# Optimization experiments

Measured on AMD Instinct MI355X. Metric: run time of the kernel, lower is better.

## Reference

```python
import jax, jax.numpy as jnp
import numpy as np

B, L, S, LA, NA, E, D, H, NHID = 16, 256, 100, 48, 32, 64, 768, 12, 1024
W_IDX = S + 2
EPS = 1e-12


def setup_inputs() -> dict:
    rng = np.random.default_rng(0)
    key = jax.random.key(0)
    ks = jax.random.split(key, 8)
    idxs = np.zeros((B, W_IDX), dtype=np.int64)
    bert_lens = np.zeros((B,), dtype=np.int64)
    is_trig = np.zeros((B, S), dtype=np.float32)
    ent_map = np.zeros((B, S, E), dtype=np.float32)
    argw_mask = np.zeros((B, LA, 1), dtype=np.float32)
    for b in range(B):
        sb = int(rng.integers(60, S + 1))          # n first-subword tokens
        ab = int(rng.integers(8, LA + 1))          # n arg-role subwords
        sent_idx = np.sort(rng.choice(np.arange(1, 2 * sb + 1), size=sb, replace=False))
        sls = 2 * sb + 1                           # second-to-last [SEP] position
        last = sls + ab + 1                        # last [SEP] position
        idxs[b, :sb] = sent_idx
        idxs[b, sb] = sls
        idxs[b, sb + 1] = last
        bert_lens[b] = last + 1
        t0 = int(rng.integers(0, sb - 1))
        is_trig[b, t0:t0 + 2] = 1.0
        eb = int(rng.integers(16, E + 1))
        for e in range(eb):
            ent_map[b, int(rng.integers(0, sb)), e] = 1.0
        argw_mask[b, :ab, 0] = 1.0
    arg_w = np.asarray(jax.random.uniform(ks[0], (B, LA, NA), dtype=jnp.float32)) * argw_mask
    return {
        'all_embeddings': jax.random.normal(ks[1], (B, L, D), dtype=jnp.float32),
        'is_triggers': jnp.asarray(is_trig),
        'arg_weight_matrices': jnp.asarray(arg_w, dtype=jnp.float32),
        'entity_mapping': jnp.asarray(ent_map),
        'att0': jax.random.uniform(ks[2], (B, H, L, L), dtype=jnp.float32),
        'att1': jax.random.uniform(ks[3], (B, H, L, L), dtype=jnp.float32),
        'att2': jax.random.uniform(ks[4], (B, H, L, L), dtype=jnp.float32),
        'W_ta': jax.random.normal(ks[5], (3 * D, D), dtype=jnp.float32) * 0.02,
        'b_ta': jnp.zeros((D,), dtype=jnp.float32),
        'W1': jax.random.normal(ks[6], (6 * D, NHID), dtype=jnp.float32) * 0.02,
        'b1': jnp.zeros((NHID,), dtype=jnp.float32),
        'W2': jax.random.normal(ks[7], (NHID, 1), dtype=jnp.float32) * 0.02,
        'b2': jnp.zeros((1,), dtype=jnp.float32),
        'idxs_to_collect': jnp.asarray(idxs),
        'bert_sentence_lengths': jnp.asarray(bert_lens),
    }


def _l1_normalize(x, axis):
    # F.normalize(x, p=1, dim=axis)
    return x / jnp.clip(jnp.sum(jnp.abs(x), axis=axis, keepdims=True), EPS)


def reference(all_embeddings, is_triggers, arg_weight_matrices, entity_mapping,
              att0, att1, att2, W_ta, b_ta, W1, b1, W2, b2,
              idxs_to_collect, bert_sentence_lengths):
    idxs = idxs_to_collect
    valid = idxs > 0                                   # [B,W]
    n_valid = jnp.sum(valid, axis=1)                   # [B]
    j = jnp.arange(S)
    sent_valid = (j[None, :] < (n_valid - 2)[:, None]).astype(all_embeddings.dtype)  # [B,S]
    sent_idx = idxs[:, :S]
    # first-subword gather, zero-padded (get_fist_subword_embeddings)
    sent_emb = jnp.take_along_axis(all_embeddings, sent_idx[:, :, None], axis=1) * sent_valid[:, :, None]
    # arg-role segment: (second_last_sep+1) .. (bert_len-2), zero-padded to LA
    sls = jnp.take_along_axis(idxs, (n_valid - 2)[:, None], axis=1)[:, 0]   # [B]
    arg_pos = sls[:, None] + 1 + jnp.arange(LA)[None, :]                    # [B,LA]
    arg_valid = (arg_pos < (bert_sentence_lengths - 1)[:, None]).astype(all_embeddings.dtype)
    arg_emb0 = jnp.take_along_axis(all_embeddings, jnp.clip(arg_pos, 0, L - 1)[:, :, None], axis=1) * arg_valid[:, :, None]
    # entity aggregation + trigger mean pooling
    entity = jnp.einsum('bsd,bse->bed', sent_emb, entity_mapping)           # [B,E,D]
    trig = jnp.sum(sent_emb * is_triggers[:, :, None], axis=1) / jnp.sum(is_triggers, axis=1)[:, None]
    arg = jnp.einsum('bld,bla->bad', arg_emb0, arg_weight_matrices)         # [B,NA,D]
    # trigger-aware entity fusion
    trig_e = jnp.broadcast_to(trig[:, None, :], entity.shape)
    nonempty = (jnp.sum(jnp.abs(entity), axis=-1) > 0).astype(entity.dtype)
    ent_cat = jnp.concatenate([entity, trig_e, entity * trig_e], axis=-1)   # [B,E,3D]
    entity = (ent_cat @ W_ta + b_ta) * nonempty[:, :, None]
    # bidirectional token<->arg attention (L1-normalized)
    score = jnp.einsum('bed,bad->bea', entity, arg) / np.sqrt(D)            # [B,E,NA]
    t2a = _l1_normalize(score, 2)[..., None]
    a2t = _l1_normalize(score, 1)[..., None]
    token_argAwared = jnp.sum(arg[:, None] * t2a, axis=2)                   # [B,E,D]
    arg_tokenAwared = jnp.sum(entity[:, :, None] * a2t, axis=1)             # [B,NA,D]
    # select_hidden_att: head-mean, gather collected rows/cols, row-renormalize
    def sel_att(att):
        m = jnp.mean(att, axis=1)                                           # [B,L,L]
        r = jnp.take_along_axis(m, sent_idx[:, :, None], axis=1)            # [B,S,L]
        c = jnp.take_along_axis(r, sent_idx[:, None, :], axis=2)            # [B,S,S]
        c = c * sent_valid[:, :, None] * sent_valid[:, None, :]
        return c / jnp.clip(jnp.sum(c, axis=-1, keepdims=True), EPS)
    t2t = (sel_att(att0) + sel_att(att1) + sel_att(att2)) / 3.0             # [B,S,S]
    a_h2h_tok = t2t @ sent_emb                                              # [B,S,D]
    A_h2h = jnp.einsum('bse,bsd->bed', entity_mapping, a_h2h_tok)           # [B,E,D]
    H_ = jnp.einsum('bse,bsd->bed', entity_mapping, sent_emb)               # [B,E,D]
    a2a = jax.nn.softmax(arg @ jnp.swapaxes(arg, -1, -2), axis=-1)
    A_u2u = a2a @ arg                                                       # [B,NA,D]
    shp = (B, E, NA, D)
    latent = jnp.concatenate([
        jnp.broadcast_to(H_[:, :, None], shp),
        jnp.broadcast_to(arg[:, None], shp),
        jnp.broadcast_to(token_argAwared[:, :, None], shp),
        jnp.broadcast_to(A_h2h[:, :, None], shp),
        jnp.broadcast_to(arg_tokenAwared[:, None], shp),
        jnp.broadcast_to(A_u2u[:, None], shp),
    ], axis=-1)                                                             # [B,E,NA,6D]
    h = jax.nn.gelu(latent @ W1 + b1, approximate=False)
    out = (h @ W2 + b2)[..., 0]                                             # [B,E,NA]
    return out
```

## Files before the change

kernel.cpp:

```cpp
#include <hip/hip_runtime.h>
#include <math.h>

#define B_ 16
#define L_ 256
#define S_ 100
#define LA_ 48
#define NA_ 32
#define E_ 64
#define D_ 768
#define H_ 12
#define NHID_ 1024
#define WIDX_ 102
#define EPSF 1e-12f

typedef __attribute__((ext_vector_type(8))) short s16x8;
typedef __attribute__((ext_vector_type(4))) float f32x4;

__device__ __forceinline__ void split_bf16(float x, unsigned short& h, unsigned short& l) {
  unsigned u = __float_as_uint(x);
  unsigned hr = u + 0x7FFFu + ((u >> 16) & 1u);
  h = (unsigned short)(hr >> 16);
  float r = x - __uint_as_float(hr & 0xFFFF0000u);
  unsigned u2 = __float_as_uint(r);
  unsigned lr = u2 + 0x7FFFu + ((u2 >> 16) & 1u);
  l = (unsigned short)(lr >> 16);
}

__global__ void k_meta(const int* __restrict__ idxs, const int* __restrict__ blen,
                       int* __restrict__ meta) {
  int b = blockIdx.x, t = threadIdx.x;
  __shared__ int cnt;
  if (t == 0) cnt = 0;
  __syncthreads();
  if (t < WIDX_ && idxs[b * WIDX_ + t] > 0) atomicAdd(&cnt, 1);
  __syncthreads();
  if (t == 0) {
    int sb = cnt - 2;
    meta[b * 4 + 0] = sb;
    meta[b * 4 + 1] = idxs[b * WIDX_ + sb];
    meta[b * 4 + 2] = blen[b] - 1;
  }
}

__global__ void k_gather(const float* __restrict__ emb, const int* __restrict__ idxs,
                         const int* __restrict__ meta, float* __restrict__ sent_emb,
                         float* __restrict__ arg_emb) {
  int b = blockIdx.y, y = blockIdx.x, t = threadIdx.x;
  int sb = meta[b * 4 + 0], sls = meta[b * 4 + 1], last = meta[b * 4 + 2];
  if (y < S_) {
    int s = y;
    float* dst = sent_emb + ((size_t)b * S_ + s) * D_;
    if (s < sb) {
      const float* src = emb + ((size_t)b * L_ + idxs[b * WIDX_ + s]) * D_;
      for (int d = t; d < D_; d += 256) dst[d] = src[d];
    } else {
      for (int d = t; d < D_; d += 256) dst[d] = 0.f;
    }
  } else {
    int l = y - S_;
    int pos = sls + 1 + l;
    float* dst = arg_emb + ((size_t)b * LA_ + l) * D_;
    if (pos < last) {
      int p = pos > (L_ - 1) ? (L_ - 1) : pos;
      const float* src = emb + ((size_t)b * L_ + p) * D_;
      for (int d = t; d < D_; d += 256) dst[d] = src[d];
    } else {
      for (int d = t; d < D_; d += 256) dst[d] = 0.f;
    }
  }
}

__global__ void k_trig(const float* __restrict__ sent_emb, const float* __restrict__ is_trig,
                       float* __restrict__ trig) {
  int b = blockIdx.y;
  int d = blockIdx.x * 256 + threadIdx.x;
  float acc = 0.f, den = 0.f;
  for (int s = 0; s < S_; s++) {
    float w = is_trig[b * S_ + s];
    den += w;
    if (w != 0.f) acc += w * sent_emb[((size_t)b * S_ + s) * D_ + d];
  }
  trig[b * D_ + d] = acc / den;
}

__global__ __launch_bounds__(256) void k_entity0(const float* __restrict__ sent_emb,
                                                 const float* __restrict__ ent_map,
                                                 const float* __restrict__ trig,
                                                 unsigned short* __restrict__ e0h,
                                                 unsigned short* __restrict__ e0l,
                                                 unsigned short* __restrict__ e0th,
                                                 unsigned short* __restrict__ e0tl,
                                                 float* __restrict__ ne) {
  int b = blockIdx.y, e = blockIdx.x, t = threadIdx.x;
  float a0 = 0.f, a1 = 0.f, a2 = 0.f;
  for (int s = 0; s < S_; s++) {
    float w = ent_map[((size_t)b * S_ + s) * E_ + e];
    if (w != 0.f) {
      const float* r = sent_emb + ((size_t)b * S_ + s) * D_;
      a0 += w * r[t]; a1 += w * r[t + 256]; a2 += w * r[t + 512];
    }
  }
  size_t o = ((size_t)b * E_ + e) * D_;
  const float* tr = trig + b * D_;
  unsigned short h, lo;
  split_bf16(a0, h, lo); e0h[o + t] = h; e0l[o + t] = lo;
  split_bf16(a1, h, lo); e0h[o + t + 256] = h; e0l[o + t + 256] = lo;
  split_bf16(a2, h, lo); e0h[o + t + 512] = h; e0l[o + t + 512] = lo;
  split_bf16(a0 * tr[t], h, lo); e0th[o + t] = h; e0tl[o + t] = lo;
  split_bf16(a1 * tr[t + 256], h, lo); e0th[o + t + 256] = h; e0tl[o + t + 256] = lo;
  split_bf16(a2 * tr[t + 512], h, lo); e0th[o + t + 512] = h; e0tl[o + t + 512] = lo;
  __shared__ float red[256];
  red[t] = fabsf(a0) + fabsf(a1) + fabsf(a2);
  __syncthreads();
  for (int s2 = 128; s2 > 0; s2 >>= 1) {
    if (t < s2) red[t] += red[t + s2];
    __syncthreads();
  }
  if (t == 0) ne[b * E_ + e] = (red[0] > 0.f) ? 1.f : 0.f;
}

__global__ __launch_bounds__(256) void k_wsum(const float* __restrict__ Wm, int wstride, int sy,
                                              int sx, const float* __restrict__ Vm,
                                              float* __restrict__ Om,
                                              unsigned short* __restrict__ oh,
                                              unsigned short* __restrict__ ol, int Y) {
  int b = blockIdx.y, x = blockIdx.x, t = threadIdx.x;
  float a0 = 0.f, a1 = 0.f, a2 = 0.f;
  const float* wb = Wm + (size_t)b * wstride + (size_t)x * sx;
  const float* vb = Vm + (size_t)b * Y * D_;
  for (int y = 0; y < Y; y++) {
    float w = wb[(size_t)y * sy];
    if (w != 0.f) {
      const float* r = vb + (size_t)y * D_;
      a0 += w * r[t]; a1 += w * r[t + 256]; a2 += w * r[t + 512];
    }
  }
  size_t oidx = ((size_t)b * gridDim.x + x) * D_;
  if (Om) {
    Om[oidx + t] = a0; Om[oidx + t + 256] = a1; Om[oidx + t + 512] = a2;
  }
  if (oh) {
    unsigned short h, lo;
    split_bf16(a0, h, lo); oh[oidx + t] = h; ol[oidx + t] = lo;
    split_bf16(a1, h, lo); oh[oidx + t + 256] = h; ol[oidx + t + 256] = lo;
    split_bf16(a2, h, lo); oh[oidx + t + 512] = h; ol[oidx + t + 512] = lo;
  }
}

__global__ void k_tb(const float* __restrict__ trig, const float* __restrict__ W_ta,
                     const float* __restrict__ b_ta, float* __restrict__ tb) {
  int b = blockIdx.y;
  int d = blockIdx.x * 256 + threadIdx.x;
  float acc0 = b_ta[d], acc1 = 0.f, acc2 = 0.f, acc3 = 0.f;
  float acc4 = 0.f, acc5 = 0.f, acc6 = 0.f, acc7 = 0.f;
  const float* tr = trig + b * D_;
  const float* w = W_ta + (size_t)D_ * D_ + d;
  for (int k = 0; k < D_; k += 8) {
    acc0 += tr[k + 0] * w[(size_t)(k + 0) * D_];
    acc1 += tr[k + 1] * w[(size_t)(k + 1) * D_];
    acc2 += tr[k + 2] * w[(size_t)(k + 2) * D_];
    acc3 += tr[k + 3] * w[(size_t)(k + 3) * D_];
    acc4 += tr[k + 4] * w[(size_t)(k + 4) * D_];
    acc5 += tr[k + 5] * w[(size_t)(k + 5) * D_];
    acc6 += tr[k + 6] * w[(size_t)(k + 6) * D_];
    acc7 += tr[k + 7] * w[(size_t)(k + 7) * D_];
  }
  tb[b * D_ + d] = ((acc0 + acc1) + (acc2 + acc3)) + ((acc4 + acc5) + (acc6 + acc7));
}

__global__ __launch_bounds__(256) void k_cvtT(const float* __restrict__ src, int K, int N,
                                              unsigned short* __restrict__ th,
                                              unsigned short* __restrict__ tl) {
  __shared__ float tile[32][33];
  int k0 = blockIdx.x * 32, n0 = blockIdx.y * 32;
  int tr = threadIdx.x >> 3, c4 = (threadIdx.x & 7) * 4;
  float4 v = *(const float4*)(src + (size_t)(k0 + tr) * N + n0 + c4);
  tile[tr][c4] = v.x; tile[tr][c4 + 1] = v.y; tile[tr][c4 + 2] = v.z; tile[tr][c4 + 3] = v.w;
  __syncthreads();
  unsigned short h[4], l[4];
#pragma unroll
  for (int i = 0; i < 4; ++i) split_bf16(tile[c4 + i][tr], h[i], l[i]);
  size_t oo = (size_t)(n0 + tr) * K + k0 + c4;
  th[oo + 0] = h[0]; th[oo + 1] = h[1]; th[oo + 2] = h[2]; th[oo + 3] = h[3];
  tl[oo + 0] = l[0]; tl[oo + 1] = l[1]; tl[oo + 2] = l[2]; tl[oo + 3] = l[3];
}

__global__ __launch_bounds__(256) void k_mgemm(
    int phase,
    const unsigned short* __restrict__ e0h, const unsigned short* __restrict__ e0l,
    const unsigned short* __restrict__ e0th, const unsigned short* __restrict__ e0tl,
    const unsigned short* __restrict__ Ah2hh, const unsigned short* __restrict__ Ah2hl,
    const unsigned short* __restrict__ argmh, const unsigned short* __restrict__ argml,
    const unsigned short* __restrict__ Au2uh, const unsigned short* __restrict__ Au2ul,
    const unsigned short* __restrict__ entnh, const unsigned short* __restrict__ entnl,
    const unsigned short* __restrict__ WtaTh, const unsigned short* __restrict__ WtaTl,
    const unsigned short* __restrict__ W1Th, const unsigned short* __restrict__ W1Tl,
    float* __restrict__ Cpe, float* __restrict__ PeAp, float* __restrict__ PaAp,
    float* __restrict__ P2, float* __restrict__ Q2) {
  const size_t HPE = (size_t)B_ * E_ * NHID_;
  const size_t HPA = (size_t)B_ * NA_ * NHID_;
  const size_t HH = (size_t)1024 * 768;
  int flat = blockIdx.x;
  int xcd = flat & 7;
  int i = flat >> 3;
  int by8 = i & 7;
  int colIdx = i >> 3;
  int job, bx, byTop = 0;
  if (phase == 0) {
    int gc = xcd * 20 + colIdx;
    if (gc < 24)       { job = 0; int r = gc;       bx = r >> 1; byTop = (r & 1) << 3; }
    else if (gc < 48)  { job = 1; int r = gc - 24;  bx = r >> 1; byTop = (r & 1) << 3; }
    else if (gc < 80)  { job = 2; int r = gc - 48;  bx = r >> 1; byTop = (r & 1) << 3; }
    else if (gc < 112) { job = 3; int r = gc - 80;  bx = r >> 1; byTop = (r & 1) << 3; }
    else if (gc < 128) { job = 4; bx = gc - 112; }
    else if (gc < 144) { job = 5; bx = gc - 128; }
    else               { job = 6; bx = gc - 144; }
  } else {
    int gc = xcd * 4 + colIdx;
    job = 7; bx = gc >> 1; byTop = (gc & 1) << 3;
  }
  int by = byTop + by8;

  const unsigned short *Ah_, *Al_, *Bh_, *Bl_;
  float* C;
  int bstride, N, bkoff;
  switch (job) {
    case 0: Ah_ = e0h;   Al_ = e0l;   Bh_ = WtaTh; Bl_ = WtaTl; bstride = 2304;
            bkoff = 0;        C = Cpe;        N = 768;  break;
    case 1: Ah_ = e0th;  Al_ = e0tl;  Bh_ = WtaTh; Bl_ = WtaTl; bstride = 2304;
            bkoff = 1536;     C = Cpe + HH;   N = 768;  break;
    case 2: Ah_ = e0h;   Al_ = e0l;   Bh_ = W1Th;  Bl_ = W1Tl;  bstride = 4608;
            bkoff = 0;        C = PeAp;       N = 1024; break;
    case 3: Ah_ = Ah2hh; Al_ = Ah2hl; Bh_ = W1Th;  Bl_ = W1Tl;  bstride = 4608;
            bkoff = 3 * 768;  C = PeAp + HPE; N = 1024; break;
    case 4: Ah_ = argmh; Al_ = argml; Bh_ = W1Th;  Bl_ = W1Tl;  bstride = 4608;
            bkoff = 768;      C = PaAp;       N = 1024; break;
    case 5: Ah_ = Au2uh; Al_ = Au2ul; Bh_ = W1Th;  Bl_ = W1Tl;  bstride = 4608;
            bkoff = 5 * 768;  C = PaAp + HPA; N = 1024; break;
    case 6: Ah_ = argmh; Al_ = argml; Bh_ = W1Th;  Bl_ = W1Tl;  bstride = 4608;
            bkoff = 2 * 768;  C = P2;         N = 1024; break;
    default: Ah_ = entnh; Al_ = entnl; Bh_ = W1Th; Bl_ = W1Tl;  bstride = 4608;
            bkoff = 4 * 768;  C = Q2;         N = 1024; break;
  }

  __shared__ unsigned short As[2][2][64][4][8];
  __shared__ unsigned short Bs[2][2][64][4][8];

  int tid = threadIdx.x;
  int srow = tid >> 2, sg = tid & 3;
  int wc = sg ^ ((srow >> 1) & 3);
  const unsigned short* aPh = Ah_ + (size_t)(by * 64 + srow) * 768 + sg * 8;
  const unsigned short* aPl = Al_ + (size_t)(by * 64 + srow) * 768 + sg * 8;
  const unsigned short* bPh = Bh_ + (size_t)(bx * 64 + srow) * bstride + bkoff + sg * 8;
  const unsigned short* bPl = Bl_ + (size_t)(bx * 64 + srow) * bstride + bkoff + sg * 8;

  int lane = tid & 63, wave = tid >> 6;
  int wm = wave >> 1, wn = wave & 1;
  int fg = lane >> 4, fr = lane & 15;
  int ar0 = wm * 32 + fr;
  int bc0 = wn * 32 + fr;
  int ca = fg ^ ((ar0 >> 1) & 3);
  int cb = fg ^ ((bc0 >> 1) & 3);

  f32x4 acc00 = {0.f, 0.f, 0.f, 0.f}, acc01 = {0.f, 0.f, 0.f, 0.f};
  f32x4 acc10 = {0.f, 0.f, 0.f, 0.f}, acc11 = {0.f, 0.f, 0.f, 0.f};

  const int niter = 24;
  s16x8 a0h = *(const s16x8*)(aPh + 0), a0l = *(const s16x8*)(aPl + 0);
  s16x8 b0h = *(const s16x8*)(bPh + 0), b0l = *(const s16x8*)(bPl + 0);
  s16x8 a1h = *(const s16x8*)(aPh + 32), a1l = *(const s16x8*)(aPl + 32);
  s16x8 b1h = *(const s16x8*)(bPh + 32), b1l = *(const s16x8*)(bPl + 32);

#define WRITE_LDS(buf, ah, al, bh, bl)              \
  {                                                 \
    *(s16x8*)&As[buf][0][srow][wc][0] = ah;         \
    *(s16x8*)&As[buf][1][srow][wc][0] = al;         \
    *(s16x8*)&Bs[buf][0][srow][wc][0] = bh;         \
    *(s16x8*)&Bs[buf][1][srow][wc][0] = bl;         \
  }
#define LOAD_SET(ah, al, bh, bl, t_)                \
  {                                                 \
    ah = *(const s16x8*)(aPh + (t_) * 32);          \
    al = *(const s16x8*)(aPl + (t_) * 32);          \
    bh = *(const s16x8*)(bPh + (t_) * 32);          \
    bl = *(const s16x8*)(bPl + (t_) * 32);          \
  }
#define READ_MFMA(buf)                                                          \
  {                                                                             \
    s16x8 xah0 = *(const s16x8*)&As[buf][0][ar0][ca][0];                        \
    s16x8 xah1 = *(const s16x8*)&As[buf][0][ar0 + 16][ca][0];                   \
    s16x8 xal0 = *(const s16x8*)&As[buf][1][ar0][ca][0];                        \
    s16x8 xal1 = *(const s16x8*)&As[buf][1][ar0 + 16][ca][0];                   \
    s16x8 xbh0 = *(const s16x8*)&Bs[buf][0][bc0][cb][0];                        \
    s16x8 xbh1 = *(const s16x8*)&Bs[buf][0][bc0 + 16][cb][0];                   \
    s16x8 xbl0 = *(const s16x8*)&Bs[buf][1][bc0][cb][0];                        \
    s16x8 xbl1 = *(const s16x8*)&Bs[buf][1][bc0 + 16][cb][0];                   \
    acc00 = __builtin_amdgcn_mfma_f32_16x16x32_bf16(xah0, xbh0, acc00, 0, 0, 0); \
    acc00 = __builtin_amdgcn_mfma_f32_16x16x32_bf16(xah0, xbl0, acc00, 0, 0, 0); \
    acc00 = __builtin_amdgcn_mfma_f32_16x16x32_bf16(xal0, xbh0, acc00, 0, 0, 0); \
    acc01 = __builtin_amdgcn_mfma_f32_16x16x32_bf16(xah0, xbh1, acc01, 0, 0, 0); \
    acc01 = __builtin_amdgcn_mfma_f32_16x16x32_bf16(xah0, xbl1, acc01, 0, 0, 0); \
    acc01 = __builtin_amdgcn_mfma_f32_16x16x32_bf16(xal0, xbh1, acc01, 0, 0, 0); \
    acc10 = __builtin_amdgcn_mfma_f32_16x16x32_bf16(xah1, xbh0, acc10, 0, 0, 0); \
    acc10 = __builtin_amdgcn_mfma_f32_16x16x32_bf16(xah1, xbl0, acc10, 0, 0, 0); \
    acc10 = __builtin_amdgcn_mfma_f32_16x16x32_bf16(xal1, xbh0, acc10, 0, 0, 0); \
    acc11 = __builtin_amdgcn_mfma_f32_16x16x32_bf16(xah1, xbh1, acc11, 0, 0, 0); \
    acc11 = __builtin_amdgcn_mfma_f32_16x16x32_bf16(xah1, xbl1, acc11, 0, 0, 0); \
    acc11 = __builtin_amdgcn_mfma_f32_16x16x32_bf16(xal1, xbh1, acc11, 0, 0, 0); \
  }

  WRITE_LDS(0, a0h, a0l, b0h, b0l);
  LOAD_SET(a0h, a0l, b0h, b0l, 2);
  __syncthreads();

  for (int it = 0; it < niter; it += 2) {
    if (it + 1 < niter) {
      WRITE_LDS(1, a1h, a1l, b1h, b1l);
      if (it + 3 < niter) LOAD_SET(a1h, a1l, b1h, b1l, it + 3);
    }
    READ_MFMA(0);
    __syncthreads();
    if (it + 2 < niter) {
      WRITE_LDS(0, a0h, a0l, b0h, b0l);
      if (it + 4 < niter) LOAD_SET(a0h, a0l, b0h, b0l, it + 4);
    }
    READ_MFMA(1);
    __syncthreads();
  }
#undef WRITE_LDS
#undef LOAD_SET
#undef READ_MFMA

  f32x4 accs[2][2] = {{acc00, acc01}, {acc10, acc11}};
  int colb = bx * 64 + wn * 32 + fr;
  int rowb = by * 64 + wm * 32 + fg * 4;
#pragma unroll
  for (int i2 = 0; i2 < 2; ++i2) {
#pragma unroll
    for (int j = 0; j < 2; ++j) {
      int col = colb + j * 16;
#pragma unroll
      for (int r = 0; r < 4; ++r) {
        int row = rowb + i2 * 16 + r;
        C[(size_t)row * N + col] = accs[i2][j][r];
      }
    }
  }
}

__global__ __launch_bounds__(256) void k_combE(const float* __restrict__ Cpe,
                                               const float* __restrict__ tb,
                                               const float* __restrict__ ne,
                                               float* __restrict__ entn,
                                               unsigned short* __restrict__ entnh,
                                               unsigned short* __restrict__ entnl) {
  int t = threadIdx.x;
  int r0 = blockIdx.x * 4;
  const size_t HH = (size_t)1024 * 768;
#pragma unroll
  for (int i = 0; i < 4; ++i) {
    int row = r0 + i;
    int b = row >> 6;
    float nev = ne[row];
#pragma unroll
    for (int j = 0; j < 3; ++j) {
      int col = t + j * 256;
      size_t o = (size_t)row * D_ + col;
      float v = (Cpe[o] + Cpe[HH + o] + tb[(size_t)b * D_ + col]) * nev;
      entn[o] = v;
      unsigned short hh, ll;
      split_bf16(v, hh, ll);
      entnh[o] = hh; entnl[o] = ll;
    }
  }
}

__global__ __launch_bounds__(256) void k_score(const float* __restrict__ entn,
                                               const float* __restrict__ argm,
                                               float* __restrict__ score) {
  int b = blockIdx.y, e = blockIdx.x, t = threadIdx.x;
  __shared__ float ent[D_];
  const float* er = entn + ((size_t)b * E_ + e) * D_;
  for (int d = t; d < D_; d += 256) ent[d] = er[d];
  __syncthreads();
  int wave = t >> 6, lane = t & 63;
  const float scale = 0.03608439182435161f;
  for (int a = wave; a < NA_; a += 4) {
    const float* ar = argm + ((size_t)b * NA_ + a) * D_;
    float p = 0.f;
#pragma unroll
    for (int i = 0; i < 12; i++) {
      int d = lane + 64 * i;
      p += ent[d] * ar[d];
    }
    for (int off = 32; off > 0; off >>= 1) p += __shfl_down(p, off);
    if (lane == 0) score[((size_t)b * E_ + e) * NA_ + a] = p * scale;
  }
}

__global__ __launch_bounds__(256) void k_a2a(const float* __restrict__ argm,
                                             float* __restrict__ a2a) {
  int b = blockIdx.y, a = blockIdx.x, t = threadIdx.x;
  __shared__ float sA[D_];
  __shared__ float lg[NA_];
  const float* ar = argm + ((size_t)b * NA_ + a) * D_;
  for (int d = t; d < D_; d += 256) sA[d] = ar[d];
  __syncthreads();
  int wave = t >> 6, lane = t & 63;
  for (int a2 = wave; a2 < NA_; a2 += 4) {
    const float* br = argm + ((size_t)b * NA_ + a2) * D_;
    float p = 0.f;
#pragma unroll
    for (int i = 0; i < 12; i++) {
      int d = lane + 64 * i;
      p += sA[d] * br[d];
    }
    for (int off = 32; off > 0; off >>= 1) p += __shfl_down(p, off);
    if (lane == 0) lg[a2] = p;
  }
  __syncthreads();
  if (t < 64) {
    float v = (t < NA_) ? lg[t] : -INFINITY;
    float m = v;
    for (int mask = 16; mask > 0; mask >>= 1) m = fmaxf(m, __shfl_xor(m, mask));
    float ex = (t < NA_) ? expf(v - m) : 0.f;
    float sm = ex;
    for (int mask = 16; mask > 0; mask >>= 1) sm += __shfl_xor(sm, mask);
    if (t < NA_) a2a[((size_t)b * NA_ + a) * NA_ + t] = ex / sm;
  }
}

__global__ __launch_bounds__(128) void k_t2t(const float* __restrict__ att0,
                                             const float* __restrict__ att1,
                                             const float* __restrict__ att2,
                                             const int* __restrict__ idxs,
                                             const int* __restrict__ meta,
                                             float* __restrict__ t2t) {
  int b = blockIdx.y, s = blockIdx.x, t = threadIdx.x;
  int sb = meta[b * 4 + 0];
  float* out = t2t + ((size_t)b * S_ + s) * S_;
  if (s >= sb) {
    for (int j = t; j < S_; j += 128) out[j] = 0.f;
    return;
  }
  int Is = idxs[b * WIDX_ + s];
  int It = (t < S_) ? idxs[b * WIDX_ + t] : 0;
  __shared__ float row[256];
  __shared__ float red[128];
  const float* atts[3] = {att0, att1, att2};
  float accout = 0.f;
  for (int q = 0; q < 3; q++) {
    float r0 = 0.f, r1 = 0.f;
    const float* base = atts[q] + (((size_t)b * H_) * L_ + Is) * L_;
    for (int h = 0; h < H_; h++) {
      const float* rp = base + (size_t)h * L_ * L_;
      r0 += rp[t];
      r1 += rp[t + 128];
    }
    row[t] = r0;
    row[t + 128] = r1;
    __syncthreads();
    float v = (t < sb) ? row[It] * (1.f / 12.f) : 0.f;
    red[t] = v;
    __syncthreads();
    for (int s2 = 64; s2 > 0; s2 >>= 1) {
      if (t < s2) red[t] += red[t + s2];
      __syncthreads();
    }
    float rsum = red[0];
    __syncthreads();
    accout += v / fmaxf(rsum, EPSF) * (1.f / 3.f);
  }
  if (t < S_) out[t] = accout;
}

__global__ __launch_bounds__(256) void k_mix(const float* __restrict__ PeAp,
                                             const float* __restrict__ PaAp,
                                             const float* __restrict__ P2,
                                             const float* __restrict__ Q2,
                                             const float* __restrict__ score,
                                             const float* __restrict__ b1,
                                             float* __restrict__ ps, float* __restrict__ qs) {
  int b = blockIdx.y, x = blockIdx.x, t = threadIdx.x;
  int n0 = t * 4;
  const size_t HPE = (size_t)B_ * E_ * NHID_;
  const size_t HPA = (size_t)B_ * NA_ * NHID_;
  __shared__ float sc[E_];
  if (x < E_) {
    int e = x;
    size_t ro = ((size_t)b * E_ + e) * NHID_ + n0;
    float4 acc = *(const float4*)(PeAp + ro);
    float4 u1 = *(const float4*)(PeAp + HPE + ro);
    float4 bb = *(const float4*)(b1 + n0);
    acc.x += u1.x + bb.x; acc.y += u1.y + bb.y;
    acc.z += u1.z + bb.z; acc.w += u1.w + bb.w;
    if (t < NA_) sc[t] = score[((size_t)b * E_ + e) * NA_ + t];
    __syncthreads();
    float rs = 0.f;
    for (int a = 0; a < NA_; a++) rs += fabsf(sc[a]);
    rs = fmaxf(rs, EPSF);
    const float* pb = P2 + (size_t)b * NA_ * NHID_ + n0;
#pragma unroll 2
    for (int a = 0; a < NA_; a++) {
      float ww = sc[a] / rs;
      float4 p = *(const float4*)(pb + (size_t)a * NHID_);
      acc.x += ww * p.x; acc.y += ww * p.y; acc.z += ww * p.z; acc.w += ww * p.w;
    }
    *(float4*)(ps + ro) = acc;
  } else {
    int a = x - E_;
    size_t ro = ((size_t)b * NA_ + a) * NHID_ + n0;
    float4 acc = *(const float4*)(PaAp + ro);
    float4 u1 = *(const float4*)(PaAp + HPA + ro);
    acc.x += u1.x; acc.y += u1.y; acc.z += u1.z; acc.w += u1.w;
    if (t < E_) sc[t] = score[((size_t)b * E_ + t) * NA_ + a];
    __syncthreads();
    float cs = 0.f;
    for (int e = 0; e < E_; e++) cs += fabsf(sc[e]);
    cs = fmaxf(cs, EPSF);
    const float* qb = Q2 + (size_t)b * E_ * NHID_ + n0;
#pragma unroll 2
    for (int e = 0; e < E_; e++) {
      float ww = sc[e] / cs;
      float4 q = *(const float4*)(qb + (size_t)e * NHID_);
      acc.x += ww * q.x; acc.y += ww * q.y; acc.z += ww * q.z; acc.w += ww * q.w;
    }
    *(float4*)(qs + ro) = acc;
  }
}

__global__ __launch_bounds__(256) void k_final(const float* __restrict__ ps,
                                               const float* __restrict__ qs,
                                               const float* __restrict__ W2,
                                               const float* __restrict__ b2,
                                               float* __restrict__ out) {
  int b = blockIdx.y, e = blockIdx.x, t = threadIdx.x;
  int wave = t >> 6, lane = t & 63;
  const float ks = 0.70710678118654752f;
  size_t po = ((size_t)b * E_ + e) * NHID_ + lane * 4;
  float4 p0 = *(const float4*)(ps + po);
  float4 p1 = *(const float4*)(ps + po + 256);
  float4 p2 = *(const float4*)(ps + po + 512);
  float4 p3 = *(const float4*)(ps + po + 768);
  const float* w2p = W2 + lane * 4;
  float4 w0 = *(const float4*)(w2p);
  float4 w1 = *(const float4*)(w2p + 256);
  float4 w2 = *(const float4*)(w2p + 512);
  float4 w3 = *(const float4*)(w2p + 768);
  __shared__ float outs[NA_];
#pragma unroll 2
  for (int a = wave; a < NA_; a += 4) {
    size_t qo = ((size_t)b * NA_ + a) * NHID_ + lane * 4;
    float4 q0 = *(const float4*)(qs + qo);
    float4 q1 = *(const float4*)(qs + qo + 256);
    float4 q2 = *(const float4*)(qs + qo + 512);
    float4 q3 = *(const float4*)(qs + qo + 768);
    float acc = 0.f;
#define GEL4(pp, qq, ww)                                          \
    {                                                             \
      float x0 = pp.x + qq.x, x1 = pp.y + qq.y;                   \
      float x2 = pp.z + qq.z, x3 = pp.w + qq.w;                   \
      float g0 = 0.5f * x0 * (1.f + erff(x0 * ks));               \
      float g1 = 0.5f * x1 * (1.f + erff(x1 * ks));               \
      float g2 = 0.5f * x2 * (1.f + erff(x2 * ks));               \
      float g3 = 0.5f * x3 * (1.f + erff(x3 * ks));               \
      acc += g0 * ww.x + g1 * ww.y + g2 * ww.z + g3 * ww.w;       \
    }
    GEL4(p0, q0, w0)
    GEL4(p1, q1, w1)
    GEL4(p2, q2, w2)
    GEL4(p3, q3, w3)
#undef GEL4
    acc += __shfl_xor(acc, 32);
    acc += __shfl_xor(acc, 16);
    acc += __shfl_xor(acc, 8);
    acc += __shfl_xor(acc, 4);
    acc += __shfl_xor(acc, 2);
    acc += __shfl_xor(acc, 1);
    if (lane == 0) outs[a] = acc;
  }
  __syncthreads();
  if (t < NA_) out[((size_t)b * E_ + e) * NA_ + t] = outs[t] + b2[0];
}

extern "C" void kernel_launch(void* const* d_in, const int* in_sizes, int n_in,
                              void* d_out, int out_size, void* d_ws, size_t ws_size,
                              hipStream_t stream) {
  const float* emb    = (const float*)d_in[0];
  const float* istrig = (const float*)d_in[1];
  const float* argw   = (const float*)d_in[2];
  const float* entmap = (const float*)d_in[3];
  const float* att0   = (const float*)d_in[4];
  const float* att1   = (const float*)d_in[5];
  const float* att2   = (const float*)d_in[6];
  const float* W_ta   = (const float*)d_in[7];
  const float* b_ta   = (const float*)d_in[8];
  const float* W1     = (const float*)d_in[9];
  const float* b1     = (const float*)d_in[10];
  const float* W2     = (const float*)d_in[11];
  const float* b2     = (const float*)d_in[12];
  const int*   idxs   = (const int*)d_in[13];
  const int*   blen   = (const int*)d_in[14];
  float* out = (float*)d_out;

  float* ws = (float*)d_ws;
  size_t o = 0;
  int* meta = (int*)ws; o += 256;
  float* sent_emb = ws + o; o += (size_t)B_ * S_ * D_;
  float* arg_emb  = ws + o; o += (size_t)B_ * LA_ * D_;
  float* trig     = ws + o; o += (size_t)B_ * D_;
  float* argm     = ws + o; o += (size_t)B_ * NA_ * D_;
  float* entn     = ws + o; o += (size_t)B_ * E_ * D_;
  float* tb       = ws + o; o += (size_t)B_ * D_;
  float* ne       = ws + o; o += (size_t)B_ * E_;
  float* score    = ws + o; o += (size_t)B_ * E_ * NA_;
  float* t2t      = ws + o; o += (size_t)B_ * S_ * S_;
  float* ah2h     = ws + o; o += (size_t)B_ * S_ * D_;
  float* a2a      = ws + o; o += (size_t)B_ * NA_ * NA_;
  float* Cpe      = ws + o; o += (size_t)2 * 1024 * 768;
  float* PeAp     = ws + o; o += (size_t)2 * B_ * E_ * NHID_;
  float* PaAp     = ws + o; o += (size_t)2 * B_ * NA_ * NHID_;
  float* P2       = ws + o; o += (size_t)B_ * NA_ * NHID_;
  float* Q2       = ws + o; o += (size_t)B_ * E_ * NHID_;
  float* ps = sent_emb;
  float* qs = arg_emb;

  o = (o + 3) & ~(size_t)3;
  unsigned short* us = (unsigned short*)(ws + o);
  size_t uo = 0;
  unsigned short* e0h   = us + uo; uo += (size_t)B_ * E_ * D_;
  unsigned short* e0l   = us + uo; uo += (size_t)B_ * E_ * D_;
  unsigned short* e0th  = us + uo; uo += (size_t)B_ * E_ * D_;
  unsigned short* e0tl  = us + uo; uo += (size_t)B_ * E_ * D_;
  unsigned short* Ah2hh = us + uo; uo += (size_t)B_ * E_ * D_;
  unsigned short* Ah2hl = us + uo; uo += (size_t)B_ * E_ * D_;
  unsigned short* argmh = us + uo; uo += (size_t)B_ * NA_ * D_;
  unsigned short* argml = us + uo; uo += (size_t)B_ * NA_ * D_;
  unsigned short* Au2uh = us + uo; uo += (size_t)B_ * NA_ * D_;
  unsigned short* Au2ul = us + uo; uo += (size_t)B_ * NA_ * D_;
  unsigned short* entnh = us + uo; uo += (size_t)B_ * E_ * D_;
  unsigned short* entnl = us + uo; uo += (size_t)B_ * E_ * D_;
  unsigned short* WtaTh = us + uo; uo += (size_t)2304 * 768;
  unsigned short* WtaTl = us + uo; uo += (size_t)2304 * 768;
  unsigned short* W1Th  = us + uo; uo += (size_t)4608 * 1024;
  unsigned short* W1Tl  = us + uo; uo += (size_t)4608 * 1024;

  k_meta<<<B_, 128, 0, stream>>>(idxs, blen, meta);
  k_cvtT<<<dim3(2304 / 32, 768 / 32), 256, 0, stream>>>(W_ta, 2304, 768, WtaTh, WtaTl);
  k_cvtT<<<dim3(4608 / 32, 1024 / 32), 256, 0, stream>>>(W1, 4608, 1024, W1Th, W1Tl);
  k_gather<<<dim3(S_ + LA_, B_), 256, 0, stream>>>(emb, idxs, meta, sent_emb, arg_emb);
  k_trig<<<dim3(3, B_), 256, 0, stream>>>(sent_emb, istrig, trig);
  k_entity0<<<dim3(E_, B_), 256, 0, stream>>>(sent_emb, entmap, trig, e0h, e0l, e0th, e0tl, ne);
  k_wsum<<<dim3(NA_, B_), 256, 0, stream>>>(argw, LA_ * NA_, NA_, 1, arg_emb, argm, argmh,
                                            argml, LA_);
  k_tb<<<dim3(3, B_), 256, 0, stream>>>(trig, W_ta, b_ta, tb);
  k_t2t<<<dim3(S_, B_), 128, 0, stream>>>(att0, att1, att2, idxs, meta, t2t);
  k_wsum<<<dim3(S_, B_), 256, 0, stream>>>(t2t, S_ * S_, 1, S_, sent_emb, ah2h, nullptr,
                                           nullptr, S_);
  k_wsum<<<dim3(E_, B_), 256, 0, stream>>>(entmap, S_ * E_, E_, 1, ah2h, nullptr, Ah2hh,
                                           Ah2hl, S_);
  k_a2a<<<dim3(NA_, B_), 256, 0, stream>>>(argm, a2a);
  k_wsum<<<dim3(NA_, B_), 256, 0, stream>>>(a2a, NA_ * NA_, 1, NA_, argm, nullptr, Au2uh,
                                            Au2ul, NA_);

  k_mgemm<<<dim3(1280), 256, 0, stream>>>(0, e0h, e0l, e0th, e0tl, Ah2hh, Ah2hl, argmh,
                                          argml, Au2uh, Au2ul, entnh, entnl, WtaTh, WtaTl,
                                          W1Th, W1Tl, Cpe, PeAp, PaAp, P2, Q2);

  k_combE<<<dim3(B_ * E_ / 4), 256, 0, stream>>>(Cpe, tb, ne, entn, entnh, entnl);

  k_mgemm<<<dim3(256), 256, 0, stream>>>(1, e0h, e0l, e0th, e0tl, Ah2hh, Ah2hl, argmh,
                                         argml, Au2uh, Au2ul, entnh, entnl, WtaTh, WtaTl,
                                         W1Th, W1Tl, Cpe, PeAp, PaAp, P2, Q2);

  k_score<<<dim3(E_, B_), 256, 0, stream>>>(entn, argm, score);
  k_mix<<<dim3(E_ + NA_, B_), 256, 0, stream>>>(PeAp, PaAp, P2, Q2, score, b1, ps, qs);

  k_final<<<dim3(E_, B_), 256, 0, stream>>>(ps, qs, W2, b2, out);
}
```

Before: 491.0 us.

## Enlarge mgemm tiles to 128x128 and split-K the phase-1 GEMM

The split-bf16 MFMA GEMM kernel moves from 64x64 tiles, with four 16x16 accumulators per wave, to 128x128 tiles with a 4x4 accumulator grid per wave. This raises data reuse per LDS load and cuts the phase-0 grid from 1280 blocks to 320. Phase 1 (entity GEMM) is split along K into two halves written to separate buffers, which k_mix now sums, so the small phase-1 grid still has 128 blocks. The costs are more registers and LDS per block (launch_bounds asks for 2 blocks/CU), fewer blocks to fill the GPU, and an extra Q2 buffer and read.

```diff
diff --git a/kernel.cpp b/kernel.cpp
--- a/kernel.cpp
+++ b/kernel.cpp
@@ -185,7 +185,7 @@
   tl[oo + 0] = l[0]; tl[oo + 1] = l[1]; tl[oo + 2] = l[2]; tl[oo + 3] = l[3];
 }
 
-__global__ __launch_bounds__(256) void k_mgemm(
+__global__ __launch_bounds__(256, 2) void k_mgemm(
     int phase,
     const unsigned short* __restrict__ e0h, const unsigned short* __restrict__ e0l,
     const unsigned short* __restrict__ e0th, const unsigned short* __restrict__ e0tl,
@@ -203,146 +203,152 @@
   int flat = blockIdx.x;
   int xcd = flat & 7;
   int i = flat >> 3;
-  int by8 = i & 7;
-  int colIdx = i >> 3;
-  int job, bx, byTop = 0;
-  if (phase == 0) {
-    int gc = xcd * 20 + colIdx;
-    if (gc < 24)       { job = 0; int r = gc;       bx = r >> 1; byTop = (r & 1) << 3; }
-    else if (gc < 48)  { job = 1; int r = gc - 24;  bx = r >> 1; byTop = (r & 1) << 3; }
-    else if (gc < 80)  { job = 2; int r = gc - 48;  bx = r >> 1; byTop = (r & 1) << 3; }
-    else if (gc < 112) { job = 3; int r = gc - 80;  bx = r >> 1; byTop = (r & 1) << 3; }
-    else if (gc < 128) { job = 4; bx = gc - 112; }
-    else if (gc < 144) { job = 5; bx = gc - 128; }
-    else               { job = 6; bx = gc - 144; }
-  } else {
-    int gc = xcd * 4 + colIdx;
-    job = 7; bx = gc >> 1; byTop = (gc & 1) << 3;
-  }
-  int by = byTop + by8;
-
+  int by4 = i & 3;
+  int seg = i >> 2;
+  int job, bx, byTop = 0, akoff = 0, niter, bkoff, bstride, N;
   const unsigned short *Ah_, *Al_, *Bh_, *Bl_;
   float* C;
-  int bstride, N, bkoff;
-  switch (job) {
-    case 0: Ah_ = e0h;   Al_ = e0l;   Bh_ = WtaTh; Bl_ = WtaTl; bstride = 2304;
-            bkoff = 0;        C = Cpe;        N = 768;  break;
-    case 1: Ah_ = e0th;  Al_ = e0tl;  Bh_ = WtaTh; Bl_ = WtaTl; bstride = 2304;
-            bkoff = 1536;     C = Cpe + HH;   N = 768;  break;
-    case 2: Ah_ = e0h;   Al_ = e0l;   Bh_ = W1Th;  Bl_ = W1Tl;  bstride = 4608;
-            bkoff = 0;        C = PeAp;       N = 1024; break;
-    case 3: Ah_ = Ah2hh; Al_ = Ah2hl; Bh_ = W1Th;  Bl_ = W1Tl;  bstride = 4608;
-            bkoff = 3 * 768;  C = PeAp + HPE; N = 1024; break;
-    case 4: Ah_ = argmh; Al_ = argml; Bh_ = W1Th;  Bl_ = W1Tl;  bstride = 4608;
-            bkoff = 768;      C = PaAp;       N = 1024; break;
-    case 5: Ah_ = Au2uh; Al_ = Au2ul; Bh_ = W1Th;  Bl_ = W1Tl;  bstride = 4608;
-            bkoff = 5 * 768;  C = PaAp + HPA; N = 1024; break;
-    case 6: Ah_ = argmh; Al_ = argml; Bh_ = W1Th;  Bl_ = W1Tl;  bstride = 4608;
-            bkoff = 2 * 768;  C = P2;         N = 1024; break;
-    default: Ah_ = entnh; Al_ = entnl; Bh_ = W1Th; Bl_ = W1Tl;  bstride = 4608;
-            bkoff = 4 * 768;  C = Q2;         N = 1024; break;
-  }
-
-  __shared__ unsigned short As[2][2][64][4][8];
-  __shared__ unsigned short Bs[2][2][64][4][8];
+  if (phase == 0) {
+    int gseg = xcd * 10 + seg;
+    niter = 24;
+    if (gseg < 12)      { job = 0; bx = gseg >> 1;                 byTop = (gseg & 1) * 4; }
+    else if (gseg < 24) { job = 1; int r = gseg - 24 + 12; r = gseg - 12; bx = r >> 1; byTop = (r & 1) * 4; }
+    else if (gseg < 40) { job = 2; int r = gseg - 24; bx = r >> 1; byTop = (r & 1) * 4; }
+    else if (gseg < 56) { job = 3; int r = gseg - 40; bx = r >> 1; byTop = (r & 1) * 4; }
+    else if (gseg < 64) { job = 4; bx = gseg - 56; }
+    else if (gseg < 72) { job = 5; bx = gseg - 64; }
+    else                { job = 6; bx = gseg - 72; }
+    switch (job) {
+      case 0: Ah_ = e0h;   Al_ = e0l;   Bh_ = WtaTh; Bl_ = WtaTl; bstride = 2304;
+              bkoff = 0;        C = Cpe;        N = 768;  break;
+      case 1: Ah_ = e0th;  Al_ = e0tl;  Bh_ = WtaTh; Bl_ = WtaTl; bstride = 2304;
+              bkoff = 1536;     C = Cpe + HH;   N = 1024; N = 768; break;
+      case 2: Ah_ = e0h;   Al_ = e0l;   Bh_ = W1Th;  Bl_ = W1Tl;  bstride = 4608;
+              bkoff = 0;        C = PeAp;       N = 1024; break;
+      case 3: Ah_ = Ah2hh; Al_ = Ah2hl; Bh_ = W1Th;  Bl_ = W1Tl;  bstride = 4608;
+              bkoff = 3 * 768;  C = PeAp + HPE; N = 1024; break;
+      case 4: Ah_ = argmh; Al_ = argml; Bh_ = W1Th;  Bl_ = W1Tl;  bstride = 4608;
+              bkoff = 768;      C = PaAp;       N = 1024; break;
+      case 5: Ah_ = Au2uh; Al_ = Au2ul; Bh_ = W1Th;  Bl_ = W1Tl;  bstride = 4608;
+              bkoff = 5 * 768;  C = PaAp + HPA; N = 1024; break;
+      default: Ah_ = argmh; Al_ = argml; Bh_ = W1Th; Bl_ = W1Tl;  bstride = 4608;
+              bkoff = 2 * 768;  C = P2;         N = 1024; break;
+    }
+  } else {
+    int gseg = xcd * 4 + seg;
+    int kh = gseg & 1;
+    int ck = gseg >> 1;
+    bx = ck >> 1; byTop = (ck & 1) * 4;
+    niter = 12; akoff = kh * 384;
+    Ah_ = entnh; Al_ = entnl; Bh_ = W1Th; Bl_ = W1Tl; bstride = 4608;
+    bkoff = 4 * 768 + kh * 384; C = Q2 + (size_t)kh * HPE; N = 1024;
+  }
+  int by = byTop + by4;
+
+  __shared__ unsigned short As[2][2][128][4][8];
+  __shared__ unsigned short Bs[2][2][128][4][8];
 
   int tid = threadIdx.x;
   int srow = tid >> 2, sg = tid & 3;
   int wc = sg ^ ((srow >> 1) & 3);
-  const unsigned short* aPh = Ah_ + (size_t)(by * 64 + srow) * 768 + sg * 8;
-  const unsigned short* aPl = Al_ + (size_t)(by * 64 + srow) * 768 + sg * 8;
-  const unsigned short* bPh = Bh_ + (size_t)(bx * 64 + srow) * bstride + bkoff + sg * 8;
-  const unsigned short* bPl = Bl_ + (size_t)(bx * 64 + srow) * bstride + bkoff + sg * 8;
+  const unsigned short* aPh0 = Ah_ + (size_t)(by * 128 + srow) * 768 + akoff + sg * 8;
+  const unsigned short* aPl0 = Al_ + (size_t)(by * 128 + srow) * 768 + akoff + sg * 8;
+  const unsigned short* bPh0 = Bh_ + (size_t)(bx * 128 + srow) * bstride + bkoff + sg * 8;
+  const unsigned short* bPl0 = Bl_ + (size_t)(bx * 128 + srow) * bstride + bkoff + sg * 8;
+  const size_t aRo = (size_t)64 * 768;
+  const size_t bRo = (size_t)64 * bstride;
 
   int lane = tid & 63, wave = tid >> 6;
   int wm = wave >> 1, wn = wave & 1;
   int fg = lane >> 4, fr = lane & 15;
-  int ar0 = wm * 32 + fr;
-  int bc0 = wn * 32 + fr;
+  int ar0 = wm * 64 + fr;
+  int bc0 = wn * 64 + fr;
   int ca = fg ^ ((ar0 >> 1) & 3);
   int cb = fg ^ ((bc0 >> 1) & 3);
 
-  f32x4 acc00 = {0.f, 0.f, 0.f, 0.f}, acc01 = {0.f, 0.f, 0.f, 0.f};
-  f32x4 acc10 = {0.f, 0.f, 0.f, 0.f}, acc11 = {0.f, 0.f, 0.f, 0.f};
-
-  const int niter = 24;
-  s16x8 a0h = *(const s16x8*)(aPh + 0), a0l = *(const s16x8*)(aPl + 0);
-  s16x8 b0h = *(const s16x8*)(bPh + 0), b0l = *(const s16x8*)(bPl + 0);
-  s16x8 a1h = *(const s16x8*)(aPh + 32), a1l = *(const s16x8*)(aPl + 32);
-  s16x8 b1h = *(const s16x8*)(bPh + 32), b1l = *(const s16x8*)(bPl + 32);
-
-#define WRITE_LDS(buf, ah, al, bh, bl)              \
-  {                                                 \
-    *(s16x8*)&As[buf][0][srow][wc][0] = ah;         \
-    *(s16x8*)&As[buf][1][srow][wc][0] = al;         \
-    *(s16x8*)&Bs[buf][0][srow][wc][0] = bh;         \
-    *(s16x8*)&Bs[buf][1][srow][wc][0] = bl;         \
-  }
-#define LOAD_SET(ah, al, bh, bl, t_)                \
-  {                                                 \
-    ah = *(const s16x8*)(aPh + (t_) * 32);          \
-    al = *(const s16x8*)(aPl + (t_) * 32);          \
-    bh = *(const s16x8*)(bPh + (t_) * 32);          \
-    bl = *(const s16x8*)(bPl + (t_) * 32);          \
-  }
-#define READ_MFMA(buf)                                                          \
-  {                                                                             \
-    s16x8 xah0 = *(const s16x8*)&As[buf][0][ar0][ca][0];                        \
-    s16x8 xah1 = *(const s16x8*)&As[buf][0][ar0 + 16][ca][0];                   \
-    s16x8 xal0 = *(const s16x8*)&As[buf][1][ar0][ca][0];                        \
-    s16x8 xal1 = *(const s16x8*)&As[buf][1][ar0 + 16][ca][0];                   \
-    s16x8 xbh0 = *(const s16x8*)&Bs[buf][0][bc0][cb][0];                        \
-    s16x8 xbh1 = *(const s16x8*)&Bs[buf][0][bc0 + 16][cb][0];                   \
-    s16x8 xbl0 = *(const s16x8*)&Bs[buf][1][bc0][cb][0];                        \
-    s16x8 xbl1 = *(const s16x8*)&Bs[buf][1][bc0 + 16][cb][0];                   \
-    acc00 = __builtin_amdgcn_mfma_f32_16x16x32_bf16(xah0, xbh0, acc00, 0, 0, 0); \
-    acc00 = __builtin_amdgcn_mfma_f32_16x16x32_bf16(xah0, xbl0, acc00, 0, 0, 0); \
-    acc00 = __builtin_amdgcn_mfma_f32_16x16x32_bf16(xal0, xbh0, acc00, 0, 0, 0); \
-    acc01 = __builtin_amdgcn_mfma_f32_16x16x32_bf16(xah0, xbh1, acc01, 0, 0, 0); \
-    acc01 = __builtin_amdgcn_mfma_f32_16x16x32_bf16(xah0, xbl1, acc01, 0, 0, 0); \
-    acc01 = __builtin_amdgcn_mfma_f32_16x16x32_bf16(xal0, xbh1, acc01, 0, 0, 0); \
-    acc10 = __builtin_amdgcn_mfma_f32_16x16x32_bf16(xah1, xbh0, acc10, 0, 0, 0); \
-    acc10 = __builtin_amdgcn_mfma_f32_16x16x32_bf16(xah1, xbl0, acc10, 0, 0, 0); \
-    acc10 = __builtin_amdgcn_mfma_f32_16x16x32_bf16(xal1, xbh0, acc10, 0, 0, 0); \
-    acc11 = __builtin_amdgcn_mfma_f32_16x16x32_bf16(xah1, xbh1, acc11, 0, 0, 0); \
-    acc11 = __builtin_amdgcn_mfma_f32_16x16x32_bf16(xah1, xbl1, acc11, 0, 0, 0); \
-    acc11 = __builtin_amdgcn_mfma_f32_16x16x32_bf16(xal1, xbh1, acc11, 0, 0, 0); \
-  }
-
-  WRITE_LDS(0, a0h, a0l, b0h, b0l);
-  LOAD_SET(a0h, a0l, b0h, b0l, 2);
-  __syncthreads();
-
-  for (int it = 0; it < niter; it += 2) {
+  f32x4 acc[4][4];
+#pragma unroll
+  for (int ii = 0; ii < 4; ++ii)
+#pragma unroll
+    for (int jj = 0; jj < 4; ++jj) acc[ii][jj] = (f32x4){0.f, 0.f, 0.f, 0.f};
+
+  s16x8 rA0h = *(const s16x8*)(aPh0);
+  s16x8 rA0l = *(const s16x8*)(aPl0);
+  s16x8 rA1h = *(const s16x8*)(aPh0 + aRo);
+  s16x8 rA1l = *(const s16x8*)(aPl0 + aRo);
+  s16x8 rB0h = *(const s16x8*)(bPh0);
+  s16x8 rB0l = *(const s16x8*)(bPl0);
+  s16x8 rB1h = *(const s16x8*)(bPh0 + bRo);
+  s16x8 rB1l = *(const s16x8*)(bPl0 + bRo);
+
+#define WRITE_LDS(buf)                                    \
+  {                                                       \
+    *(s16x8*)&As[buf][0][srow][wc][0] = rA0h;             \
+    *(s16x8*)&As[buf][0][srow + 64][wc][0] = rA1h;        \
+    *(s16x8*)&As[buf][1][srow][wc][0] = rA0l;             \
+    *(s16x8*)&As[buf][1][srow + 64][wc][0] = rA1l;        \
+    *(s16x8*)&Bs[buf][0][srow][wc][0] = rB0h;             \
+    *(s16x8*)&Bs[buf][0][srow + 64][wc][0] = rB1h;        \
+    *(s16x8*)&Bs[buf][1][srow][wc][0] = rB0l;             \
+    *(s16x8*)&Bs[buf][1][srow + 64][wc][0] = rB1l;        \
+  }
+#define LOAD_SET(t_)                                      \
+  {                                                       \
+    rA0h = *(const s16x8*)(aPh0 + (t_) * 32);             \
+    rA0l = *(const s16x8*)(aPl0 + (t_) * 32);             \
+    rA1h = *(const s16x8*)(aPh0 + aRo + (t_) * 32);       \
+    rA1l = *(const s16x8*)(aPl0 + aRo + (t_) * 32);       \
+    rB0h = *(const s16x8*)(bPh0 + (t_) * 32);             \
+    rB0l = *(const s16x8*)(bPl0 + (t_) * 32);             \
+    rB1h = *(const s16x8*)(bPh0 + bRo + (t_) * 32);       \
+    rB1l = *(const s16x8*)(bPl0 + bRo + (t_) * 32);       \
+  }
+
+  WRITE_LDS(0);
+  LOAD_SET(1);
+  __syncthreads();
+
+  for (int it = 0; it < niter; ++it) {
+    int buf = it & 1;
     if (it + 1 < niter) {
-      WRITE_LDS(1, a1h, a1l, b1h, b1l);
-      if (it + 3 < niter) LOAD_SET(a1h, a1l, b1h, b1l, it + 3);
-    }
-    READ_MFMA(0);
-    __syncthreads();
-    if (it + 2 < niter) {
-      WRITE_LDS(0, a0h, a0l, b0h, b0l);
-      if (it + 4 < niter) LOAD_SET(a0h, a0l, b0h, b0l, it + 4);
-    }
-    READ_MFMA(1);
+      WRITE_LDS(buf ^ 1);
+      if (it + 2 < niter) LOAD_SET(it + 2);
+    }
+    {
+      s16x8 ah[4], al[4], bh[4], bl[4];
+#pragma unroll
+      for (int g = 0; g < 4; ++g) {
+        ah[g] = *(const s16x8*)&As[buf][0][ar0 + g * 16][ca][0];
+        al[g] = *(const s16x8*)&As[buf][1][ar0 + g * 16][ca][0];
+        bh[g] = *(const s16x8*)&Bs[buf][0][bc0 + g * 16][cb][0];
+        bl[g] = *(const s16x8*)&Bs[buf][1][bc0 + g * 16][cb][0];
+      }
+#pragma unroll
+      for (int ii = 0; ii < 4; ++ii) {
+#pragma unroll
+        for (int jj = 0; jj < 4; ++jj) {
+          acc[ii][jj] = __builtin_amdgcn_mfma_f32_16x16x32_bf16(ah[ii], bh[jj], acc[ii][jj], 0, 0, 0);
+          acc[ii][jj] = __builtin_amdgcn_mfma_f32_16x16x32_bf16(ah[ii], bl[jj], acc[ii][jj], 0, 0, 0);
+          acc[ii][jj] = __builtin_amdgcn_mfma_f32_16x16x32_bf16(al[ii], bh[jj], acc[ii][jj], 0, 0, 0);
+        }
+      }
+    }
     __syncthreads();
   }
 #undef WRITE_LDS
 #undef LOAD_SET
-#undef READ_MFMA
-
-  f32x4 accs[2][2] = {{acc00, acc01}, {acc10, acc11}};
-  int colb = bx * 64 + wn * 32 + fr;
-  int rowb = by * 64 + wm * 32 + fg * 4;
-#pragma unroll
-  for (int i2 = 0; i2 < 2; ++i2) {
-#pragma unroll
-    for (int j = 0; j < 2; ++j) {
-      int col = colb + j * 16;
+
+  int colb = bx * 128 + wn * 64 + fr;
+  int rowb = by * 128 + wm * 64 + fg * 4;
+#pragma unroll
+  for (int ii = 0; ii < 4; ++ii) {
+#pragma unroll
+    for (int jj = 0; jj < 4; ++jj) {
+      int col = colb + jj * 16;
 #pragma unroll
       for (int r = 0; r < 4; ++r) {
-        int row = rowb + i2 * 16 + r;
-        C[(size_t)row * N + col] = accs[i2][j][r];
+        int row = rowb + ii * 16 + r;
+        C[(size_t)row * N + col] = acc[ii][jj][r];
       }
     }
   }
@@ -477,7 +483,7 @@
 __global__ __launch_bounds__(256) void k_mix(const float* __restrict__ PeAp,
                                              const float* __restrict__ PaAp,
                                              const float* __restrict__ P2,
-                                             const float* __restrict__ Q2,
+                                             const float* __restrict__ Q2p,
                                              const float* __restrict__ score,
                                              const float* __restrict__ b1,
                                              float* __restrict__ ps, float* __restrict__ qs) {
@@ -518,12 +524,14 @@
     float cs = 0.f;
     for (int e = 0; e < E_; e++) cs += fabsf(sc[e]);
     cs = fmaxf(cs, EPSF);
-    const float* qb = Q2 + (size_t)b * E_ * NHID_ + n0;
+    const float* qb = Q2p + (size_t)b * E_ * NHID_ + n0;
 #pragma unroll 2
     for (int e = 0; e < E_; e++) {
       float ww = sc[e] / cs;
-      float4 q = *(const float4*)(qb + (size_t)e * NHID_);
-      acc.x += ww * q.x; acc.y += ww * q.y; acc.z += ww * q.z; acc.w += ww * q.w;
+      float4 q0v = *(const float4*)(qb + (size_t)e * NHID_);
+      float4 q1v = *(const float4*)(qb + HPE + (size_t)e * NHID_);
+      acc.x += ww * (q0v.x + q1v.x); acc.y += ww * (q0v.y + q1v.y);
+      acc.z += ww * (q0v.z + q1v.z); acc.w += ww * (q0v.w + q1v.w);
     }
     *(float4*)(qs + ro) = acc;
   }
@@ -621,7 +629,7 @@
   float* PeAp     = ws + o; o += (size_t)2 * B_ * E_ * NHID_;
   float* PaAp     = ws + o; o += (size_t)2 * B_ * NA_ * NHID_;
   float* P2       = ws + o; o += (size_t)B_ * NA_ * NHID_;
-  float* Q2       = ws + o; o += (size_t)B_ * E_ * NHID_;
+  float* Q2       = ws + o; o += (size_t)2 * B_ * E_ * NHID_;
   float* ps = sent_emb;
   float* qs = arg_emb;
 
@@ -663,16 +671,16 @@
   k_wsum<<<dim3(NA_, B_), 256, 0, stream>>>(a2a, NA_ * NA_, 1, NA_, argm, nullptr, Au2uh,
                                             Au2ul, NA_);
 
-  k_mgemm<<<dim3(1280), 256, 0, stream>>>(0, e0h, e0l, e0th, e0tl, Ah2hh, Ah2hl, argmh,
-                                          argml, Au2uh, Au2ul, entnh, entnl, WtaTh, WtaTl,
-                                          W1Th, W1Tl, Cpe, PeAp, PaAp, P2, Q2);
-
-  k_combE<<<dim3(B_ * E_ / 4), 256, 0, stream>>>(Cpe, tb, ne, entn, entnh, entnl);
-
-  k_mgemm<<<dim3(256), 256, 0, stream>>>(1, e0h, e0l, e0th, e0tl, Ah2hh, Ah2hl, argmh,
+  k_mgemm<<<dim3(320), 256, 0, stream>>>(0, e0h, e0l, e0th, e0tl, Ah2hh, Ah2hl, argmh,
                                          argml, Au2uh, Au2ul, entnh, entnl, WtaTh, WtaTl,
                                          W1Th, W1Tl, Cpe, PeAp, PaAp, P2, Q2);
 
+  k_combE<<<dim3(B_ * E_ / 4), 256, 0, stream>>>(Cpe, tb, ne, entn, entnh, entnl);
+
+  k_mgemm<<<dim3(128), 256, 0, stream>>>(1, e0h, e0l, e0th, e0tl, Ah2hh, Ah2hl, argmh,
+                                         argml, Au2uh, Au2ul, entnh, entnl, WtaTh, WtaTl,
+                                         W1Th, W1Tl, Cpe, PeAp, PaAp, P2, Q2);
+
   k_score<<<dim3(E_, B_), 256, 0, stream>>>(entn, argm, score);
   k_mix<<<dim3(E_ + NA_, B_), 256, 0, stream>>>(PeAp, PaAp, P2, Q2, score, b1, ps, qs);
 
```

Measured after the change: 500.0 us. About the same (+1.8%).
